# Performance work log

Measured on AMD Instinct MI355X. Metric: run time of the kernel, lower is better.

The kernel has to match this reference:

```python
import jax, jax.numpy as jnp
import numpy as np

B, N, D = 8, 4096, 256
H = W = 64          # grid_size = img_size // patch_size = 256 // 4
WS = 8              # swin window size
NH = 8              # swin heads
M = 16              # fno modes
E = 4               # num experts
TD = 768            # text dim
HID = 1024          # mlp hidden = 4 * D
TK = 2              # top_k


def gelu(x):
    return jax.nn.gelu(x, approximate=False)


def layernorm(x, g, b, eps=1e-5):
    mu = x.mean(-1, keepdims=True)
    var = ((x - mu) ** 2).mean(-1, keepdims=True)
    return (x - mu) * jax.lax.rsqrt(var + eps) * g + b


def fno_expert(x, w1r, w1i, w2r, w2i, conv_w, conv_b):
    # x: [B, N, D] -> grid [B, D, H, W]
    xg = x.transpose(0, 2, 1).reshape(B, D, H, W)
    xft = jnp.fft.rfft2(xg)                      # [B, D, H, W//2+1] complex64
    w1 = w1r + 1j * w1i
    w2 = w2r + 1j * w2i
    top = jnp.einsum('bixy,ioxy->boxy', xft[:, :, :M, :M], w1)
    bot = jnp.einsum('bixy,ioxy->boxy', xft[:, :, -M:, :M], w2)
    out_ft = jnp.zeros((B, D, H, W // 2 + 1), dtype=xft.dtype)
    out_ft = out_ft.at[:, :, :M, :M].set(top).at[:, :, -M:, :M].set(bot)
    x1 = jnp.fft.irfft2(out_ft, s=(H, W))        # [B, D, H, W]
    x2 = jnp.einsum('bdhw,do->bohw', xg, conv_w) + conv_b[None, :, None, None]
    out = gelu(x1 + x2)
    return out.reshape(B, D, N).transpose(0, 2, 1) + x


def mlp_expert(x, w1, b1, w2, b2):
    return gelu(x @ w1 + b1) @ w2 + b2 + x


def window_attn_expert(x, ln1_g, ln1_b, qkv_w, qkv_b, out_w, out_b,
                       ln2_g, ln2_b, mw1, mb1, mw2, mb2):
    shortcut = x
    h = layernorm(x, ln1_g, ln1_b)
    # window partition: [B,H,W,C] -> [B*nW, WS*WS, C]
    h = h.reshape(B, H // WS, WS, W // WS, WS, D)
    h = h.transpose(0, 1, 3, 2, 4, 5).reshape(-1, WS * WS, D)
    # multi-head self attention (torch nn.MultiheadAttention semantics)
    qkv = h @ qkv_w + qkv_b                      # [Bw, L, 3D]
    q, k, v = jnp.split(qkv, 3, axis=-1)
    dh = D // NH
    def heads(t):
        return t.reshape(-1, WS * WS, NH, dh).transpose(0, 2, 1, 3)
    q, k, v = heads(q), heads(k), heads(v)
    scores = jnp.einsum('whld,whmd->whlm', q, k) / jnp.sqrt(jnp.float32(dh))
    attn = jax.nn.softmax(scores, axis=-1)
    o = jnp.einsum('whlm,whmd->whld', attn, v)
    o = o.transpose(0, 2, 1, 3).reshape(-1, WS * WS, D)
    o = o @ out_w + out_b
    # window reverse
    o = o.reshape(B, H // WS, W // WS, WS, WS, D)
    o = o.transpose(0, 1, 3, 2, 4, 5).reshape(B, N, D)
    x = o + shortcut
    h2 = layernorm(x, ln2_g, ln2_b)
    return x + (gelu(h2 @ mw1 + mb1) @ mw2 + mb2)


def setup_inputs() -> dict:
    key = jax.random.key(0)
    ks = jax.random.split(key, 24)
    rn = lambda k, s: jax.random.normal(k, s, jnp.float32) * 0.02
    fscale = 1.0 / (D * D)
    ru = lambda k: jax.random.uniform(k, (D, D, M, M), jnp.float32) * fscale
    return {
        'x': jax.random.normal(ks[0], (B, N, D), jnp.float32),
        'text_embedding': jax.random.normal(ks[1], (B, TD), jnp.float32),
        'gate_w1': rn(ks[2], (D + TD, D)), 'gate_b1': jnp.zeros((D,), jnp.float32),
        'gate_w2': rn(ks[3], (D, E)), 'gate_b2': jnp.zeros((E,), jnp.float32),
        'fno_w1r': ru(ks[4]), 'fno_w1i': ru(ks[5]),
        'fno_w2r': ru(ks[6]), 'fno_w2i': ru(ks[7]),
        'fno_conv_w': rn(ks[8], (D, D)), 'fno_conv_b': jnp.zeros((D,), jnp.float32),
        'mlp1_w1': rn(ks[9], (D, HID)), 'mlp1_b1': jnp.zeros((HID,), jnp.float32),
        'mlp1_w2': rn(ks[10], (HID, D)), 'mlp1_b2': jnp.zeros((D,), jnp.float32),
        'mlp2_w1': rn(ks[11], (D, HID)), 'mlp2_b1': jnp.zeros((HID,), jnp.float32),
        'mlp2_w2': rn(ks[12], (HID, D)), 'mlp2_b2': jnp.zeros((D,), jnp.float32),
        'wa_ln1_g': jnp.ones((D,), jnp.float32), 'wa_ln1_b': jnp.zeros((D,), jnp.float32),
        'wa_qkv_w': rn(ks[13], (D, 3 * D)), 'wa_qkv_b': jnp.zeros((3 * D,), jnp.float32),
        'wa_out_w': rn(ks[14], (D, D)), 'wa_out_b': jnp.zeros((D,), jnp.float32),
        'wa_ln2_g': jnp.ones((D,), jnp.float32), 'wa_ln2_b': jnp.zeros((D,), jnp.float32),
        'wa_mlp_w1': rn(ks[15], (D, HID)), 'wa_mlp_b1': jnp.zeros((HID,), jnp.float32),
        'wa_mlp_w2': rn(ks[16], (HID, D)), 'wa_mlp_b2': jnp.zeros((D,), jnp.float32),
    }


def reference(x, text_embedding, gate_w1, gate_b1, gate_w2, gate_b2,
              fno_w1r, fno_w1i, fno_w2r, fno_w2i, fno_conv_w, fno_conv_b,
              mlp1_w1, mlp1_b1, mlp1_w2, mlp1_b2,
              mlp2_w1, mlp2_b1, mlp2_w2, mlp2_b2,
              wa_ln1_g, wa_ln1_b, wa_qkv_w, wa_qkv_b, wa_out_w, wa_out_b,
              wa_ln2_g, wa_ln2_b, wa_mlp_w1, wa_mlp_b1, wa_mlp_w2, wa_mlp_b2):
    # --- gating ---
    feat = jnp.concatenate([x.mean(axis=1), text_embedding], axis=1)  # [B, D+TD]
    logits = jax.nn.relu(feat @ gate_w1 + gate_b1) @ gate_w2 + gate_b2  # [B, E]
    top_v, top_i = jax.lax.top_k(logits, TK)
    weights = jax.nn.softmax(top_v, axis=-1)                           # [B, TK]
    # per-expert combined weight: cw[b,e] = sum_k w[b,k] * (idx[b,k]==e)
    cw = (jax.nn.one_hot(top_i, E, dtype=x.dtype) * weights[..., None]).sum(axis=1)  # [B, E]
    # --- experts (FNO, MLP, WindowAttn, MLP) ---
    e0 = fno_expert(x, fno_w1r, fno_w1i, fno_w2r, fno_w2i, fno_conv_w, fno_conv_b)
    e1 = mlp_expert(x, mlp1_w1, mlp1_b1, mlp1_w2, mlp1_b2)
    e2 = window_attn_expert(x, wa_ln1_g, wa_ln1_b, wa_qkv_w, wa_qkv_b,
                            wa_out_w, wa_out_b, wa_ln2_g, wa_ln2_b,
                            wa_mlp_w1, wa_mlp_b1, wa_mlp_w2, wa_mlp_b2)
    e3 = mlp_expert(x, mlp2_w1, mlp2_b1, mlp2_w2, mlp2_b2)
    outs = jnp.stack([e0, e1, e2, e3])                                 # [E, B, N, D]
    final = jnp.einsum('be,ebnd->bnd', cw, outs)
    return final, weights
```

## Files before the change

kernel.cpp:

```cpp
#include <hip/hip_runtime.h>
#include <math.h>


#define NB 8
#define NN 4096
#define DD 256

typedef __attribute__((ext_vector_type(8))) short bf16x8;
typedef __attribute__((ext_vector_type(4))) float f32x4;

__device__ __forceinline__ float gelu_f(float v) {
    return 0.5f * v * (1.0f + erff(v * 0.7071067811865475f));
}
__device__ __forceinline__ ushort f2bf(float f) {
    uint32_t u = __float_as_uint(f);
    uint32_t r = (u + 0x7fffu + ((u >> 16) & 1u)) >> 16;
    return (ushort)r;
}
__device__ __forceinline__ float b2f(ushort h) {
    return __uint_as_float(((uint32_t)h) << 16);
}

__global__ void k_cvt_gate(const float* __restrict__ src, ushort* __restrict__ dst,
                           float* __restrict__ gp) {
    __shared__ float4 st[4][64];
    int blk = blockIdx.x;
    int t = threadIdx.x;
    int i = blk * 256 + t;
    float4 v = ((const float4*)src)[i];
    ushort4 o;
    o.x = f2bf(v.x); o.y = f2bf(v.y); o.z = f2bf(v.z); o.w = f2bf(v.w);
    ((ushort4*)dst)[i] = o;
    st[t >> 6][t & 63] = v;
    __syncthreads();
    if (t < 64) {
        float4 a = st[0][t], b = st[1][t], c = st[2][t], d = st[3][t];
        float4 s;
        s.x = a.x + b.x + c.x + d.x;
        s.y = a.y + b.y + c.y + d.y;
        s.z = a.z + b.z + c.z + d.z;
        s.w = a.w + b.w + c.w + d.w;
        ((float4*)(gp + (size_t)blk * 256))[t] = s;
    }
}

__global__ void __launch_bounds__(256) k_gate_red(const float* __restrict__ gp,
        float* __restrict__ gp2) {
    int g = blockIdx.x;
    int t = threadIdx.x;
    const float* base = gp + ((size_t)g * 32) * 256;
    float s0 = 0.f, s1 = 0.f, s2 = 0.f, s3 = 0.f;
    #pragma unroll
    for (int k = 0; k < 32; k += 4) {
        s0 += base[(k + 0) * 256 + t];
        s1 += base[(k + 1) * 256 + t];
        s2 += base[(k + 2) * 256 + t];
        s3 += base[(k + 3) * 256 + t];
    }
    gp2[(size_t)g * 256 + t] = s0 + s1 + s2 + s3;
}

__global__ void __launch_bounds__(256) k_gate_mm(const float* __restrict__ gp2,
        const float* __restrict__ text, const float* __restrict__ w1,
        const float* __restrict__ b1, float* __restrict__ h1) {
    __shared__ float fs[1024];
    int b = blockIdx.x, t = threadIdx.x;
    const float* base = gp2 + (size_t)b * 32 * 256;
    float s = 0.f;
    #pragma unroll
    for (int j = 0; j < 32; ++j) s += base[j * 256 + t];
    fs[t] = s * (1.0f / NN);
    for (int j = t; j < 768; j += 256) fs[256 + j] = text[b * 768 + j];
    __syncthreads();
    float acc = b1[t];
    for (int k = 0; k < 1024; ++k) acc += fs[k] * w1[k * 256 + t];
    h1[b * 256 + t] = fmaxf(acc, 0.f);
}

__global__ void k_gate_top(const float* __restrict__ h1, const float* __restrict__ w2,
                           const float* __restrict__ b2, float* __restrict__ cw,
                           float* __restrict__ wout) {
    __shared__ float lg[8][4];
    int t = threadIdx.x;
    if (t < 32) {
        int b = t >> 2, e = t & 3;
        float acc = b2[e];
        const float* h = h1 + b * 256;
        for (int k = 0; k < 256; ++k) acc += h[k] * w2[k * 4 + e];
        lg[b][e] = acc;
    }
    __syncthreads();
    if (t < 8) {
        int b = t;
        float v[4];
        #pragma unroll
        for (int e = 0; e < 4; ++e) v[e] = lg[b][e];
        int i0 = 0;
        #pragma unroll
        for (int e = 1; e < 4; ++e) if (v[e] > v[i0]) i0 = e;
        int i1 = -1;
        #pragma unroll
        for (int e = 0; e < 4; ++e) {
            if (e == i0) continue;
            if (i1 < 0 || v[e] > v[i1]) i1 = e;
        }
        float v0 = v[i0], v1 = v[i1];
        float e1v = expf(v1 - v0);
        float inv = 1.0f / (1.0f + e1v);
        float w0 = inv, w1v = e1v * inv;
        wout[b * 2 + 0] = w0;
        wout[b * 2 + 1] = w1v;
        float c[4] = {0.f, 0.f, 0.f, 0.f};
        c[i0] += w0; c[i1] += w1v;
        #pragma unroll
        for (int e = 0; e < 4; ++e) cw[b * 4 + e] = c[e];
    }
}

__global__ void k_wt_all(const float* s0, const float* s1, const float* s2,
        const float* s3, const float* s4, const float* s5, const float* s6,
        const float* s7, const float* s8,
        ushort* d0, ushort* d1, ushort* d2, ushort* d3, ushort* d4,
        ushort* d5, ushort* d6, ushort* d7, ushort* d8) {
    const float* srcs[9] = {s0, s1, s2, s3, s4, s5, s6, s7, s8};
    ushort* dsts[9] = {d0, d1, d2, d3, d4, d5, d6, d7, d8};
    const int Ks[9] = {256, 1024, 256, 1024, 256, 1024, 256, 256, 256};
    const int Ns[9] = {1024, 256, 1024, 256, 1024, 256, 768, 256, 256};
    __shared__ float tile[32][33];
    int j = blockIdx.z;
    int K = Ks[j], N = Ns[j];
    int tn = N >> 5, tk = K >> 5;
    int tid = blockIdx.x;
    if (tid >= tn * tk) return;
    int n0 = (tid % tn) * 32, k0 = (tid / tn) * 32;
    const float* src = srcs[j];
    ushort* dst = dsts[j];
    int tx = threadIdx.x, ty = threadIdx.y;
    #pragma unroll
    for (int i = 0; i < 4; ++i)
        tile[ty + i * 8][tx] = src[(size_t)(k0 + ty + i * 8) * N + n0 + tx];
    __syncthreads();
    #pragma unroll
    for (int i = 0; i < 4; ++i)
        dst[(size_t)(n0 + ty + i * 8) * K + k0 + tx] = f2bf(tile[tx][ty + i * 8]);
}

template<int MODE>
__global__ void __launch_bounds__(256) k_gemm(const ushort* __restrict__ A,
        const ushort* __restrict__ Bt, const float* __restrict__ bias,
        const void* __restrict__ res, float* __restrict__ outf,
        ushort* __restrict__ outb, const float* __restrict__ cw, int eidx,
        int K, int Ncols, size_t bsA, size_t bsB, size_t bsC,
        const ushort* __restrict__ e0p, const ushort* __restrict__ g1p,
        const ushort* __restrict__ g2p, const ushort* __restrict__ xap) {
    __shared__ alignas(16) char smem[34816];
    ushort* sA = (ushort*)smem;
    ushort* sB = (ushort*)(smem + 16384);
    int z = blockIdx.z;
    A += z * bsA; Bt += z * bsB;
    if (outf) outf += z * bsC;
    if (outb) outb += z * bsC;
    int m0 = blockIdx.x * 128;
    int n0 = blockIdx.y * 128;
    int t = threadIdx.x;
    int lane = t & 63, wid = t >> 6;
    int wr = wid >> 1, wc = wid & 1;
    int rlo = lane & 15, khi = (lane >> 4) * 8;

    auto stage = [&](int buf, int k0) {
        const ushort* Ab = A + (size_t)m0 * K + k0;
        const ushort* Bb = Bt + (size_t)n0 * K + k0;
        #pragma unroll
        for (int h = 0; h < 2; ++h) {
            int s = t + h * 256;
            int row = s >> 2, kc = (s & 3) * 8;
            __builtin_amdgcn_global_load_lds(
                (const __attribute__((address_space(1))) void*)(Ab + (size_t)row * K + kc),
                (__attribute__((address_space(3))) void*)(sA + buf * 4096 + s * 8),
                16, 0, 0);
            __builtin_amdgcn_global_load_lds(
                (const __attribute__((address_space(1))) void*)(Bb + (size_t)row * K + kc),
                (__attribute__((address_space(3))) void*)(sB + buf * 4096 + s * 8),
                16, 0, 0);
        }
    };

    f32x4 acc[4][4];
    #pragma unroll
    for (int i = 0; i < 4; ++i)
        #pragma unroll
        for (int j = 0; j < 4; ++j) acc[i][j] = (f32x4){0.f, 0.f, 0.f, 0.f};

    int KT = K >> 5;
    stage(0, 0);
    int cur = 0;
    for (int kt = 0; kt < KT; ++kt) {
        __syncthreads();
        if (kt + 1 < KT) stage(cur ^ 1, (kt + 1) << 5);
        const ushort* Ap = sA + cur * 4096;
        const ushort* Bp = sB + cur * 4096;
        bf16x8 af[4], bfr[4];
        #pragma unroll
        for (int i = 0; i < 4; ++i) {
            af[i]  = *(const bf16x8*)(Ap + (wr * 64 + i * 16 + rlo) * 32 + khi);
            bfr[i] = *(const bf16x8*)(Bp + (wc * 64 + i * 16 + rlo) * 32 + khi);
        }
        #pragma unroll
        for (int i = 0; i < 4; ++i)
            #pragma unroll
            for (int j = 0; j < 4; ++j)
                acc[i][j] = __builtin_amdgcn_mfma_f32_16x16x32_bf16(af[i], bfr[j], acc[i][j], 0, 0, 0);
        cur ^= 1;
    }

    float bj4[4];
    if constexpr (MODE != 5) {
        #pragma unroll
        for (int nt = 0; nt < 4; ++nt) bj4[nt] = bias[n0 + wc * 64 + nt * 16 + rlo];
    }

    ushort* eb = (ushort*)smem;
    __syncthreads();
    #pragma unroll
    for (int mt = 0; mt < 4; ++mt) {
        int row0 = wr * 64 + mt * 16 + (lane >> 4) * 4;
        #pragma unroll
        for (int nt = 0; nt < 4; ++nt) {
            int col = wc * 64 + nt * 16 + rlo;
            #pragma unroll
            for (int j = 0; j < 4; ++j) {
                float v = acc[mt][nt][j];
                if constexpr (MODE == 5)
                    v += bias[m0 + row0 + j];
                else
                    v += bj4[nt];
                if (MODE == 0) v = gelu_f(v);
                eb[(row0 + j) * 136 + col] = f2bf(v);
            }
        }
    }
    __syncthreads();
    const ushort* resb = (const ushort*)res;
    #pragma unroll
    for (int h = 0; h < 8; ++h) {
        int s = t + h * 256;
        int r = s >> 4, c = (s & 15) * 8;
        int grow = m0 + r;
        size_t off = (size_t)grow * Ncols + n0 + c;
        if constexpr (MODE == 6) {
            ushort ee[8], rr[8], oo[8];
            *(uint4*)ee = *(uint4*)&eb[r * 136 + c];
            *(uint4*)rr = *(const uint4*)(resb + off);
            #pragma unroll
            for (int q = 0; q < 8; ++q) oo[q] = f2bf(b2f(ee[q]) + b2f(rr[q]));
            *(uint4*)(outb + off) = *(uint4*)oo;
        } else if constexpr (MODE == 7) {
            int bb = grow >> 12;
            float c0 = cw[bb * 4 + 0], c1 = cw[bb * 4 + 1];
            float c2 = cw[bb * 4 + 2], c3 = cw[bb * 4 + 3];
            float cx = c0 + c1 + c3;
            ushort ee[8], a0[8], a1[8], a2[8], xa[8], xb[8];
            *(uint4*)ee = *(uint4*)&eb[r * 136 + c];
            *(uint4*)a0 = *(const uint4*)(e0p + off);
            *(uint4*)a1 = *(const uint4*)(g1p + off);
            *(uint4*)a2 = *(const uint4*)(g2p + off);
            *(uint4*)xa = *(const uint4*)(xap + off);
            *(uint4*)xb = *(const uint4*)(resb + off);
            float ov[8];
            #pragma unroll
            for (int q = 0; q < 8; ++q)
                ov[q] = c0 * b2f(a0[q]) + c1 * b2f(a1[q]) + c2 * (b2f(a2[q]) + b2f(xa[q]))
                      + c3 * b2f(ee[q]) + cx * b2f(xb[q]);
            *(float4*)(outf + off) = *(float4*)&ov[0];
            *(float4*)(outf + off + 4) = *(float4*)&ov[4];
        } else {
            *(uint4*)(outb + off) = *(uint4*)&eb[r * 136 + c];
        }
    }
}

__global__ void k_transpose(const ushort* __restrict__ x, ushort* __restrict__ xg) {
    __shared__ ushort tile[32][34];
    int b = blockIdx.z;
    int nt = blockIdx.x, dt = blockIdx.y;
    int tx = threadIdx.x, ty = threadIdx.y;
    const ushort* xb = x + (size_t)b * NN * DD;
    ushort* xgb = xg + (size_t)b * DD * NN;
    #pragma unroll
    for (int i = 0; i < 4; ++i) {
        int n = nt * 32 + ty + i * 8;
        tile[ty + i * 8][tx] = xb[(size_t)n * DD + dt * 32 + tx];
    }
    __syncthreads();
    #pragma unroll
    for (int i = 0; i < 4; ++i) {
        int d = dt * 32 + ty + i * 8;
        xgb[(size_t)d * NN + nt * 32 + tx] = tile[tx][ty + i * 8];
    }
}

__global__ void __launch_bounds__(256) k_rfft2(const ushort* __restrict__ xg, float* __restrict__ xft) {
    __shared__ float plane[64][65];
    __shared__ float s1re[16][66], s1im[16][66];
    __shared__ float twc[64], tws[64];
    int p = blockIdx.x;
    int t = threadIdx.x;
    int tx = t & 63, grp = t >> 6;
    const ushort* src = xg + (size_t)p * 4096;
    #pragma unroll
    for (int i = 0; i < 16; ++i) {
        int row = grp * 16 + i;
        plane[row][tx] = b2f(src[row * 64 + tx]);
    }
    if (t < 64) {
        twc[t] = cosf((float)t * (6.283185307179586f / 64.0f));
        tws[t] = sinf((float)t * (6.283185307179586f / 64.0f));
    }
    __syncthreads();
    int r = tx;
    #pragma unroll
    for (int q = 0; q < 4; ++q) {
        int kw = grp + q * 4;
        float re = 0.f, im = 0.f;
        for (int w = 0; w < 64; ++w) {
            int j = (w * kw) & 63;
            float xv = plane[r][w];
            re += xv * twc[j];
            im -= xv * tws[j];
        }
        s1re[kw][r] = re;
        s1im[kw][r] = im;
    }
    __syncthreads();
    float2* dst = (float2*)xft + (size_t)p * 512;
    #pragma unroll
    for (int q = 0; q < 2; ++q) {
        int oi = t + q * 256;
        int krow = oi >> 4, kw = oi & 15;
        int kh = krow < 16 ? krow : krow + 32;
        float re = 0.f, im = 0.f;
        for (int h = 0; h < 64; ++h) {
            int j = (h * kh) & 63;
            float c = twc[j], s = tws[j];
            float ar = s1re[kw][h], ai = s1im[kw][h];
            re += ar * c + ai * s;
            im += ai * c - ar * s;
        }
        dst[oi] = make_float2(re, im);
    }
}

__global__ void __launch_bounds__(512) k_spectral(const float* __restrict__ xft,
        const float* __restrict__ w1r, const float* __restrict__ w1i,
        const float* __restrict__ w2r, const float* __restrict__ w2i,
        float* __restrict__ part) {
    __shared__ alignas(16) ushort Wl[16 * 640];
    __shared__ alignas(16) ushort Xl[16 * 640];
    int z = blockIdx.z;
    int region = z >> 1, is = z & 1;
    const float* wrp = region ? w2r : w1r;
    const float* wip = region ? w2i : w1i;
    int xm = blockIdx.y;
    int krow = region * 16 + xm;
    int o0 = blockIdx.x * 16;
    int t = threadIdx.x;
    int wv = t >> 6, lane = t & 63;
    int rlo = lane & 15, khi = lane >> 4;
    int ibase = is * 128;

    int wy4 = t & 3, wol = (t >> 2) & 15, wi8 = t >> 6;

    f32x4 acc[2][2];
    #pragma unroll
    for (int a = 0; a < 2; ++a)
        #pragma unroll
        for (int b = 0; b < 2; ++b) acc[a][b] = (f32x4){0.f, 0.f, 0.f, 0.f};

    for (int ch = 0; ch < 4; ++ch) {
        int i0 = ibase + ch * 32;
        int ig = i0 + wi8 * 4;
        __syncthreads();
        {
            float4 f[4];
            #pragma unroll
            for (int u = 0; u < 4; ++u)
                f[u] = *(const float4*)&wrp[((size_t)(ig + u) * 256 + o0 + wol) * 256 + xm * 16 + wy4 * 4];
            #pragma unroll
            for (int yy2 = 0; yy2 < 4; ++yy2) {
                int y = wy4 * 4 + yy2;
                ushort4 pk;
                pk.x = f2bf(((const float*)&f[0])[yy2]);
                pk.y = f2bf(((const float*)&f[1])[yy2]);
                pk.z = f2bf(((const float*)&f[2])[yy2]);
                pk.w = f2bf(((const float*)&f[3])[yy2]);
                *(ushort4*)&Wl[y * 640 + wol * 40 + wi8 * 4] = pk;
            }
        }
        {
            #pragma unroll
            for (int s = 0; s < 2; ++s) {
                int m = t + s * 512;
                int y = m & 15, i4 = (m >> 4) & 7, b = (m >> 7) & 7;
                int igx = i0 + i4 * 4;
                float2 g[4];
                #pragma unroll
                for (int u = 0; u < 4; ++u)
                    g[u] = *(const float2*)&xft[(((size_t)(b * 256 + igx + u)) * 32 + krow) * 32 + y * 2];
                ushort4 re, im;
                re.x = f2bf(g[0].x); re.y = f2bf(g[1].x); re.z = f2bf(g[2].x); re.w = f2bf(g[3].x);
                im.x = f2bf(g[0].y); im.y = f2bf(g[1].y); im.z = f2bf(g[2].y); im.w = f2bf(g[3].y);
                *(ushort4*)&Xl[b * 640 + y * 40 + i4 * 4] = re;
                *(ushort4*)&Xl[(b + 8) * 640 + y * 40 + i4 * 4] = im;
            }
        }
        __syncthreads();
        #pragma unroll
        for (int yy = 0; yy < 2; ++yy) {
            int y = wv * 2 + yy;
            bf16x8 Bf = *(const bf16x8*)&Xl[rlo * 640 + y * 40 + khi * 8];
            bf16x8 Af = *(const bf16x8*)&Wl[y * 640 + rlo * 40 + khi * 8];
            acc[yy][0] = __builtin_amdgcn_mfma_f32_16x16x32_bf16(Af, Bf, acc[yy][0], 0, 0, 0);
        }
        __syncthreads();
        {
            float4 f[4];
            #pragma unroll
            for (int u = 0; u < 4; ++u)
                f[u] = *(const float4*)&wip[((size_t)(ig + u) * 256 + o0 + wol) * 256 + xm * 16 + wy4 * 4];
            #pragma unroll
            for (int yy2 = 0; yy2 < 4; ++yy2) {
                int y = wy4 * 4 + yy2;
                ushort4 pk;
                pk.x = f2bf(((const float*)&f[0])[yy2]);
                pk.y = f2bf(((const float*)&f[1])[yy2]);
                pk.z = f2bf(((const float*)&f[2])[yy2]);
                pk.w = f2bf(((const float*)&f[3])[yy2]);
                *(ushort4*)&Wl[y * 640 + wol * 40 + wi8 * 4] = pk;
            }
        }
        __syncthreads();
        #pragma unroll
        for (int yy = 0; yy < 2; ++yy) {
            int y = wv * 2 + yy;
            bf16x8 Bf = *(const bf16x8*)&Xl[rlo * 640 + y * 40 + khi * 8];
            bf16x8 Af = *(const bf16x8*)&Wl[y * 640 + rlo * 40 + khi * 8];
            acc[yy][1] = __builtin_amdgcn_mfma_f32_16x16x32_bf16(Af, Bf, acc[yy][1], 0, 0, 0);
        }
    }

    float* dp = part + (size_t)is * 4194304;
    int b = rlo & 7, hi = rlo >> 3;
    #pragma unroll
    for (int yy = 0; yy < 2; ++yy) {
        int y = wv * 2 + yy;
        #pragma unroll
        for (int j = 0; j < 4; ++j) {
            float C1 = acc[yy][0][j];
            float c2x = __shfl_xor(acc[yy][1][j], 8);
            float val = hi ? (c2x + C1) : (C1 - c2x);
            int o = o0 + khi * 4 + j;
            dp[(((size_t)(b * 256 + o) * 32 + krow) * 16 + y) * 2 + hi] = val;
        }
    }
}

__global__ void __launch_bounds__(256) k_irfft_fuse(const float* __restrict__ part,
        const ushort* __restrict__ x2t, ushort* __restrict__ tmp) {
    __shared__ float F[32][16][2];
    __shared__ float tre[16][66], tim[16][66];
    __shared__ float twc[64], tws[64];
    int p = blockIdx.x;
    int t = threadIdx.x;
    const float2* s0 = (const float2*)part + (size_t)p * 512;
    #pragma unroll
    for (int l = 0; l < 2; ++l) {
        int idx = t + l * 256;
        float2 a = s0[idx];
        float2 b2 = s0[idx + 2097152];
        ((float2*)F)[idx] = make_float2(a.x + b2.x, a.y + b2.y);
    }
    if (t < 64) {
        twc[t] = cosf((float)t * (6.283185307179586f / 64.0f));
        tws[t] = sinf((float)t * (6.283185307179586f / 64.0f));
    }
    __syncthreads();
    int h = t & 63;
    #pragma unroll
    for (int q = 0; q < 4; ++q) {
        int kw = (t >> 6) + q * 4;
        float re = 0.f, im = 0.f;
        #pragma unroll
        for (int krow = 0; krow < 32; ++krow) {
            int kh = krow < 16 ? krow : krow + 32;
            int j = (h * kh) & 63;
            float c = twc[j], s = tws[j];
            float fr = F[krow][kw][0], fi = F[krow][kw][1];
            re += fr * c - fi * s;
            im += fr * s + fi * c;
        }
        tre[kw][h] = re * (1.f / 64.f);
        tim[kw][h] = im * (1.f / 64.f);
    }
    __syncthreads();
    const ushort* x2p = x2t + (size_t)p * 4096;
    ushort* tp = tmp + (size_t)p * 4096;
    int w = t & 63;
    #pragma unroll
    for (int qq = 0; qq < 16; ++qq) {
        int qrow = (t >> 6) + qq * 4;
        float acc = tre[0][qrow];
        #pragma unroll
        for (int kw = 1; kw < 16; ++kw) {
            int j = (w * kw) & 63;
            acc += 2.f * (tre[kw][qrow] * twc[j] - tim[kw][qrow] * tws[j]);
        }
        float x1 = acc * (1.f / 64.f);
        int idx = qrow * 64 + w;
        tp[idx] = f2bf(gelu_f(x1 + b2f(x2p[idx])));
    }
}

__global__ void k_fno_final(const ushort* __restrict__ tmp, ushort* __restrict__ e0t) {
    __shared__ ushort tile[32][34];
    int b = blockIdx.z;
    int n0 = blockIdx.x * 32, d0 = blockIdx.y * 32;
    int tx = threadIdx.x, ty = threadIdx.y;
    const ushort* tb = tmp + (size_t)b * DD * NN;
    #pragma unroll
    for (int i = 0; i < 4; ++i)
        tile[ty + i * 8][tx] = tb[(size_t)(d0 + ty + i * 8) * NN + n0 + tx];
    __syncthreads();
    #pragma unroll
    for (int i = 0; i < 4; ++i) {
        int n = n0 + ty + i * 8, d = d0 + tx;
        e0t[((size_t)b * NN + n) * DD + d] = tile[tx][ty + i * 8];
    }
}

__global__ void __launch_bounds__(256) k_ln(const ushort* __restrict__ in, const float* __restrict__ g,
        const float* __restrict__ be, ushort* __restrict__ outb) {
    int row = blockIdx.x * 4 + (threadIdx.x >> 6);
    int lane = threadIdx.x & 63;
    ushort4 u = ((const ushort4*)(in + (size_t)row * 256))[lane];
    float4 v = make_float4(b2f(u.x), b2f(u.y), b2f(u.z), b2f(u.w));
    float s = v.x + v.y + v.z + v.w;
    float s2 = v.x * v.x + v.y * v.y + v.z * v.z + v.w * v.w;
    #pragma unroll
    for (int off = 32; off > 0; off >>= 1) {
        s += __shfl_down(s, off);
        s2 += __shfl_down(s2, off);
    }
    s = __shfl(s, 0); s2 = __shfl(s2, 0);
    float mu = s * (1.f / 256.f);
    float var = s2 * (1.f / 256.f) - mu * mu;
    float rstd = rsqrtf(var + 1e-5f);
    float4 gv = ((const float4*)g)[lane];
    float4 bv = ((const float4*)be)[lane];
    ushort4 ov;
    ov.x = f2bf((v.x - mu) * rstd * gv.x + bv.x);
    ov.y = f2bf((v.y - mu) * rstd * gv.y + bv.y);
    ov.z = f2bf((v.z - mu) * rstd * gv.z + bv.z);
    ov.w = f2bf((v.w - mu) * rstd * gv.w + bv.w);
    ((ushort4*)(outb + (size_t)row * 256))[lane] = ov;
}

__global__ void __launch_bounds__(256) k_window_attn(const ushort* __restrict__ qkvb,
        ushort* __restrict__ aob) {
    __shared__ ushort lds[4 * 7424];
    int t = threadIdx.x;
    int w = t >> 6, lane = t & 63;
    int wi = blockIdx.x, hh = blockIdx.y;
    int hd = hh * 4 + w;
    int b = wi >> 6, hb = (wi >> 3) & 7, wb = wi & 7;
    ushort* A = lds + w * 7424;
    ushort* Kl = A + 2560;
    ushort* Vt = A + 5120;
    int rlo = lane & 15, kq = lane >> 4;

    int tok = lane;
    int n = hb * 512 + wb * 8 + ((tok >> 3) << 6) + (tok & 7);
    const ushort* gq = qkvb + ((size_t)b * 4096 + n) * 768 + hd * 32;
    const uint4* qp = (const uint4*)gq;
    const uint4* kp = (const uint4*)(gq + 256);
    const uint4* vp = (const uint4*)(gq + 512);
    uint4 q0 = qp[0], q1 = qp[1], q2 = qp[2], q3 = qp[3];
    uint4 k0 = kp[0], k1 = kp[1], k2 = kp[2], k3 = kp[3];
    uint4 v0 = vp[0], v1 = vp[1], v2 = vp[2], v3 = vp[3];
    uint4* qr = (uint4*)(A + tok * 40);
    qr[0] = q0; qr[1] = q1; qr[2] = q2; qr[3] = q3;
    uint4* kr = (uint4*)(Kl + tok * 40);
    kr[0] = k0; kr[1] = k1; kr[2] = k2; kr[3] = k3;
    ushort vbuf[32];
    *(uint4*)&vbuf[0] = v0; *(uint4*)&vbuf[8] = v1;
    *(uint4*)&vbuf[16] = v2; *(uint4*)&vbuf[24] = v3;
    #pragma unroll
    for (int d = 0; d < 32; ++d) Vt[d * 72 + tok] = vbuf[d];
    __syncthreads();

    bf16x8 Qf[4], Kf[4];
    #pragma unroll
    for (int lt = 0; lt < 4; ++lt)
        Qf[lt] = *(const bf16x8*)(A + (lt * 16 + rlo) * 40 + kq * 8);
    #pragma unroll
    for (int mt = 0; mt < 4; ++mt)
        Kf[mt] = *(const bf16x8*)(Kl + (mt * 16 + rlo) * 40 + kq * 8);

    f32x4 S[4][4];
    #pragma unroll
    for (int lt = 0; lt < 4; ++lt)
        #pragma unroll
        for (int mt = 0; mt < 4; ++mt)
            S[lt][mt] = __builtin_amdgcn_mfma_f32_16x16x32_bf16(Qf[lt], Kf[mt],
                        (f32x4){0.f, 0.f, 0.f, 0.f}, 0, 0, 0);
    __syncthreads();

    const float scale = 0.17677669529663687f;
    float inv_[4][4];
    #pragma unroll
    for (int lt = 0; lt < 4; ++lt) {
        float m4[4], s4[4];
        #pragma unroll
        for (int j = 0; j < 4; ++j) {
            m4[j] = fmaxf(fmaxf(S[lt][0][j], S[lt][1][j]), fmaxf(S[lt][2][j], S[lt][3][j]));
        }
        #pragma unroll
        for (int off = 1; off < 16; off <<= 1)
            #pragma unroll
            for (int j = 0; j < 4; ++j) m4[j] = fmaxf(m4[j], __shfl_xor(m4[j], off));
        #pragma unroll
        for (int j = 0; j < 4; ++j) s4[j] = 0.f;
        #pragma unroll
        for (int mt = 0; mt < 4; ++mt)
            #pragma unroll
            for (int j = 0; j < 4; ++j) {
                float p = expf((S[lt][mt][j] - m4[j]) * scale);
                s4[j] += p;
                A[(lt * 16 + kq * 4 + j) * 72 + mt * 16 + rlo] = f2bf(p);
            }
        #pragma unroll
        for (int off = 1; off < 16; off <<= 1)
            #pragma unroll
            for (int j = 0; j < 4; ++j) s4[j] += __shfl_xor(s4[j], off);
        #pragma unroll
        for (int j = 0; j < 4; ++j) inv_[lt][j] = 1.0f / s4[j];
    }
    __syncthreads();

    f32x4 O[4][2];
    #pragma unroll
    for (int lt = 0; lt < 4; ++lt)
        #pragma unroll
        for (int dt = 0; dt < 2; ++dt) {
            f32x4 o = (f32x4){0.f, 0.f, 0.f, 0.f};
            #pragma unroll
            for (int mc = 0; mc < 2; ++mc) {
                bf16x8 pa = *(const bf16x8*)(A + (lt * 16 + rlo) * 72 + mc * 32 + kq * 8);
                bf16x8 vb = *(const bf16x8*)(Vt + (dt * 16 + rlo) * 72 + mc * 32 + kq * 8);
                o = __builtin_amdgcn_mfma_f32_16x16x32_bf16(pa, vb, o, 0, 0, 0);
            }
            O[lt][dt] = o;
        }
    __syncthreads();

    #pragma unroll
    for (int lt = 0; lt < 4; ++lt)
        #pragma unroll
        for (int dt = 0; dt < 2; ++dt)
            #pragma unroll
            for (int j = 0; j < 4; ++j)
                A[(lt * 16 + kq * 4 + j) * 40 + dt * 16 + rlo] = f2bf(O[lt][dt][j] * inv_[lt][j]);
    __syncthreads();
    const uint4* orow = (const uint4*)(A + lane * 40);
    uint4 o0 = orow[0], o1 = orow[1], o2 = orow[2], o3 = orow[3];
    uint4* gout = (uint4*)(aob + ((size_t)b * 4096 + n) * 256 + hd * 32);
    gout[0] = o0; gout[1] = o1; gout[2] = o2; gout[3] = o3;
}

extern "C" void kernel_launch(void* const* d_in, const int* in_sizes, int n_in,
                              void* d_out, int out_size, void* d_ws, size_t ws_size,
                              hipStream_t stream) {
    (void)in_sizes; (void)n_in; (void)out_size; (void)ws_size;
    const float* x        = (const float*)d_in[0];
    const float* text     = (const float*)d_in[1];
    const float* gate_w1  = (const float*)d_in[2];
    const float* gate_b1  = (const float*)d_in[3];
    const float* gate_w2  = (const float*)d_in[4];
    const float* gate_b2  = (const float*)d_in[5];
    const float* fno_w1r  = (const float*)d_in[6];
    const float* fno_w1i  = (const float*)d_in[7];
    const float* fno_w2r  = (const float*)d_in[8];
    const float* fno_w2i  = (const float*)d_in[9];
    const float* fno_cw   = (const float*)d_in[10];
    const float* fno_cb   = (const float*)d_in[11];
    const float* mlp1_w1  = (const float*)d_in[12];
    const float* mlp1_b1  = (const float*)d_in[13];
    const float* mlp1_w2  = (const float*)d_in[14];
    const float* mlp1_b2  = (const float*)d_in[15];
    const float* mlp2_w1  = (const float*)d_in[16];
    const float* mlp2_b1  = (const float*)d_in[17];
    const float* mlp2_w2  = (const float*)d_in[18];
    const float* mlp2_b2  = (const float*)d_in[19];
    const float* ln1_g    = (const float*)d_in[20];
    const float* ln1_b    = (const float*)d_in[21];
    const float* qkv_w    = (const float*)d_in[22];
    const float* qkv_b    = (const float*)d_in[23];
    const float* out_w    = (const float*)d_in[24];
    const float* out_b    = (const float*)d_in[25];
    const float* ln2_g    = (const float*)d_in[26];
    const float* ln2_b    = (const float*)d_in[27];
    const float* wa_w1    = (const float*)d_in[28];
    const float* wa_b1    = (const float*)d_in[29];
    const float* wa_w2    = (const float*)d_in[30];
    const float* wa_b2    = (const float*)d_in[31];

    float* ws   = (float*)d_ws;
    float* h1   = ws + 8192;
    float* cwp  = ws + 10240;
    ushort* wbf = (ushort*)(ws + 16384);
    ushort* w1aT = wbf;
    ushort* w2aT = w1aT + 262144;
    ushort* w1bT = w2aT + 262144;
    ushort* w2bT = w1bT + 262144;
    ushort* w1cT = w2bT + 262144;
    ushort* w2cT = w1cT + 262144;
    ushort* qkvT = w2cT + 262144;
    ushort* outwT = qkvT + 196608;
    ushort* convT = outwT + 65536;
    ushort* Xbf  = (ushort*)(ws + 16384 + 1048576);
    float* slotA = ws + 16384 + 1048576 + 4194304;
    float* xft   = slotA + 8388608;
    float* oft   = xft + 2097152;
    float* regD  = oft + 2097152;
    ushort* bigb = (ushort*)(regD + 8388608);
    float* gpart = oft;
    float* gp2   = regD;

    ushort* xgb   = (ushort*)slotA;
    ushort* g1b   = (ushort*)slotA;
    ushort* g2b   = (ushort*)(slotA + 4194304);
    ushort* x2tb  = (ushort*)regD;
    ushort* e0tb  = (ushort*)regD;
    ushort* scr   = (ushort*)(regD + 4194304);
    ushort* xatb  = (ushort*)xft;

    float* outp = (float*)d_out;
    float* wout = outp + (size_t)NB * NN * DD;

    k_cvt_gate<<<8192, 256, 0, stream>>>(x, Xbf, gpart);
    k_gate_red<<<256, 256, 0, stream>>>(gpart, gp2);
    k_gate_mm<<<8, 256, 0, stream>>>(gp2, text, gate_w1, gate_b1, h1);
    k_gate_top<<<1, 64, 0, stream>>>(h1, gate_w2, gate_b2, cwp, wout);

    k_wt_all<<<dim3(256, 1, 9), dim3(32, 8), 0, stream>>>(
        mlp1_w1, mlp1_w2, mlp2_w1, mlp2_w2, wa_w1, wa_w2, qkv_w, out_w, fno_cw,
        w1aT, w2aT, w1bT, w2bT, w1cT, w2cT, qkvT, outwT, convT);

    k_transpose<<<dim3(128, 8, 8), dim3(32, 8), 0, stream>>>(Xbf, xgb);
    k_rfft2<<<2048, 256, 0, stream>>>(xgb, xft);
    k_gemm<5><<<dim3(2, 32, 8), 256, 0, stream>>>(convT, Xbf, fno_cb, nullptr, nullptr,
        x2tb, nullptr, 0, 256, 4096, 0, (size_t)NN * DD, (size_t)DD * NN,
        nullptr, nullptr, nullptr, nullptr);
    k_spectral<<<dim3(16, 16, 4), 512, 0, stream>>>(xft, fno_w1r, fno_w1i, fno_w2r, fno_w2i, slotA);
    k_irfft_fuse<<<2048, 256, 0, stream>>>(slotA, x2tb, bigb);
    k_fno_final<<<dim3(128, 8, 8), dim3(32, 8), 0, stream>>>(bigb, e0tb);

    k_gemm<0><<<dim3(256, 8), 256, 0, stream>>>(Xbf, w1aT, mlp1_b1, nullptr, nullptr, bigb, nullptr, 0, 256, 1024, 0, 0, 0, nullptr, nullptr, nullptr, nullptr);
    k_gemm<1><<<dim3(256, 2), 256, 0, stream>>>(bigb, w2aT, mlp1_b2, nullptr, nullptr, g1b, nullptr, 0, 1024, 256, 0, 0, 0, nullptr, nullptr, nullptr, nullptr);

    k_ln<<<8192, 256, 0, stream>>>(Xbf, ln1_g, ln1_b, scr);
    k_gemm<1><<<dim3(256, 6), 256, 0, stream>>>(scr, qkvT, qkv_b, nullptr, nullptr, bigb, nullptr, 0, 256, 768, 0, 0, 0, nullptr, nullptr, nullptr, nullptr);
    k_window_attn<<<dim3(512, 2), 256, 0, stream>>>(bigb, scr);
    k_gemm<6><<<dim3(256, 2), 256, 0, stream>>>(scr, outwT, out_b, Xbf, nullptr, xatb, nullptr, 0, 256, 256, 0, 0, 0, nullptr, nullptr, nullptr, nullptr);
    k_ln<<<8192, 256, 0, stream>>>(xatb, ln2_g, ln2_b, scr);
    k_gemm<0><<<dim3(256, 8), 256, 0, stream>>>(scr, w1cT, wa_b1, nullptr, nullptr, bigb, nullptr, 0, 256, 1024, 0, 0, 0, nullptr, nullptr, nullptr, nullptr);
    k_gemm<1><<<dim3(256, 2), 256, 0, stream>>>(bigb, w2cT, wa_b2, nullptr, nullptr, g2b, nullptr, 0, 1024, 256, 0, 0, 0, nullptr, nullptr, nullptr, nullptr);

    k_gemm<0><<<dim3(256, 8), 256, 0, stream>>>(Xbf, w1bT, mlp2_b1, nullptr, nullptr, bigb, nullptr, 0, 256, 1024, 0, 0, 0, nullptr, nullptr, nullptr, nullptr);
    k_gemm<7><<<dim3(256, 2), 256, 0, stream>>>(bigb, w2bT, mlp2_b2, Xbf, outp, nullptr, cwp, 3, 1024, 256, 0, 0, 0, e0tb, g1b, g2b, xatb);
}
```

Before: 643.5 us.

## Fuse bf16 conversion, transpose and gate partial sums into one kernel

Merges the fp32-to-bf16 conversion, the per-batch token-sum partials for gating, and the N/D transpose for the FNO grid into a single tiled kernel. The separate transpose pass and the gate reduction kernel go away, which saves a re-read of the bf16 input and two launches. The spectral kernel's shared-memory row stride is also padded from 640 to 648 to reduce LDS bank conflicts. The fused kernel uses 32-wide scalar loads instead of float4, which may lower load efficiency. Workspace aliasing is also changed: xgb is written before k_wt_all, in the same slot as g1b.

```diff
diff --git a/kernel.cpp b/kernel.cpp
--- a/kernel.cpp
+++ b/kernel.cpp
@@ -21,54 +21,53 @@
     return __uint_as_float(((uint32_t)h) << 16);
 }
 
-__global__ void k_cvt_gate(const float* __restrict__ src, ushort* __restrict__ dst,
-                           float* __restrict__ gp) {
-    __shared__ float4 st[4][64];
-    int blk = blockIdx.x;
-    int t = threadIdx.x;
-    int i = blk * 256 + t;
-    float4 v = ((const float4*)src)[i];
-    ushort4 o;
-    o.x = f2bf(v.x); o.y = f2bf(v.y); o.z = f2bf(v.z); o.w = f2bf(v.w);
-    ((ushort4*)dst)[i] = o;
-    st[t >> 6][t & 63] = v;
-    __syncthreads();
-    if (t < 64) {
-        float4 a = st[0][t], b = st[1][t], c = st[2][t], d = st[3][t];
-        float4 s;
-        s.x = a.x + b.x + c.x + d.x;
-        s.y = a.y + b.y + c.y + d.y;
-        s.z = a.z + b.z + c.z + d.z;
-        s.w = a.w + b.w + c.w + d.w;
-        ((float4*)(gp + (size_t)blk * 256))[t] = s;
-    }
-}
-
-__global__ void __launch_bounds__(256) k_gate_red(const float* __restrict__ gp,
-        float* __restrict__ gp2) {
-    int g = blockIdx.x;
-    int t = threadIdx.x;
-    const float* base = gp + ((size_t)g * 32) * 256;
-    float s0 = 0.f, s1 = 0.f, s2 = 0.f, s3 = 0.f;
-    #pragma unroll
-    for (int k = 0; k < 32; k += 4) {
-        s0 += base[(k + 0) * 256 + t];
-        s1 += base[(k + 1) * 256 + t];
-        s2 += base[(k + 2) * 256 + t];
-        s3 += base[(k + 3) * 256 + t];
-    }
-    gp2[(size_t)g * 256 + t] = s0 + s1 + s2 + s3;
-}
-
-__global__ void __launch_bounds__(256) k_gate_mm(const float* __restrict__ gp2,
+__global__ void k_cvt_gate_t(const float* __restrict__ src, ushort* __restrict__ xbf,
+        ushort* __restrict__ xg, float* __restrict__ gp) {
+    __shared__ ushort tile[32][34];
+    __shared__ float sred[8][32];
+    int nt = blockIdx.x, dt = blockIdx.y, b = blockIdx.z;
+    int tx = threadIdx.x, ty = threadIdx.y;
+    int n0 = nt * 32, d0 = dt * 32;
+    const float* xb = src + ((size_t)b * NN + n0) * DD + d0;
+    ushort* xbb = xbf + ((size_t)b * NN + n0) * DD + d0;
+    float s = 0.f;
+    #pragma unroll
+    for (int i = 0; i < 4; ++i) {
+        int r = ty + i * 8;
+        float v = xb[(size_t)r * DD + tx];
+        ushort h = f2bf(v);
+        xbb[(size_t)r * DD + tx] = h;
+        tile[r][tx] = h;
+        s += v;
+    }
+    sred[ty][tx] = s;
+    __syncthreads();
+    ushort* xgb = xg + (size_t)b * DD * NN;
+    #pragma unroll
+    for (int i = 0; i < 4; ++i) {
+        int d = d0 + ty + i * 8;
+        xgb[(size_t)d * NN + n0 + tx] = tile[tx][ty + i * 8];
+    }
+    if (ty == 0) {
+        float tot = 0.f;
+        #pragma unroll
+        for (int j = 0; j < 8; ++j) tot += sred[j][tx];
+        gp[(((size_t)b * 8 + dt) * 128 + nt) * 32 + tx] = tot;
+    }
+}
+
+__global__ void __launch_bounds__(256) k_gate_mm(const float* __restrict__ gp,
         const float* __restrict__ text, const float* __restrict__ w1,
         const float* __restrict__ b1, float* __restrict__ h1) {
     __shared__ float fs[1024];
     int b = blockIdx.x, t = threadIdx.x;
-    const float* base = gp2 + (size_t)b * 32 * 256;
+    int dt = t >> 5, tx = t & 31;
+    const float* base = gp + ((size_t)b * 8 + dt) * 128 * 32 + tx;
     float s = 0.f;
-    #pragma unroll
-    for (int j = 0; j < 32; ++j) s += base[j * 256 + t];
+    for (int j = 0; j < 128; j += 4) {
+        s += base[(j + 0) * 32] + base[(j + 1) * 32]
+           + base[(j + 2) * 32] + base[(j + 3) * 32];
+    }
     fs[t] = s * (1.0f / NN);
     for (int j = t; j < 768; j += 256) fs[256 + j] = text[b * 768 + j];
     __syncthreads();
@@ -279,26 +278,6 @@
     }
 }
 
-__global__ void k_transpose(const ushort* __restrict__ x, ushort* __restrict__ xg) {
-    __shared__ ushort tile[32][34];
-    int b = blockIdx.z;
-    int nt = blockIdx.x, dt = blockIdx.y;
-    int tx = threadIdx.x, ty = threadIdx.y;
-    const ushort* xb = x + (size_t)b * NN * DD;
-    ushort* xgb = xg + (size_t)b * DD * NN;
-    #pragma unroll
-    for (int i = 0; i < 4; ++i) {
-        int n = nt * 32 + ty + i * 8;
-        tile[ty + i * 8][tx] = xb[(size_t)n * DD + dt * 32 + tx];
-    }
-    __syncthreads();
-    #pragma unroll
-    for (int i = 0; i < 4; ++i) {
-        int d = dt * 32 + ty + i * 8;
-        xgb[(size_t)d * NN + nt * 32 + tx] = tile[tx][ty + i * 8];
-    }
-}
-
 __global__ void __launch_bounds__(256) k_rfft2(const ushort* __restrict__ xg, float* __restrict__ xft) {
     __shared__ float plane[64][65];
     __shared__ float s1re[16][66], s1im[16][66];
@@ -354,8 +333,8 @@
         const float* __restrict__ w1r, const float* __restrict__ w1i,
         const float* __restrict__ w2r, const float* __restrict__ w2i,
         float* __restrict__ part) {
-    __shared__ alignas(16) ushort Wl[16 * 640];
-    __shared__ alignas(16) ushort Xl[16 * 640];
+    __shared__ alignas(16) ushort Wl[16 * 648];
+    __shared__ alignas(16) ushort Xl[16 * 648];
     int z = blockIdx.z;
     int region = z >> 1, is = z & 1;
     const float* wrp = region ? w2r : w1r;
@@ -393,7 +372,7 @@
                 pk.y = f2bf(((const float*)&f[1])[yy2]);
                 pk.z = f2bf(((const float*)&f[2])[yy2]);
                 pk.w = f2bf(((const float*)&f[3])[yy2]);
-                *(ushort4*)&Wl[y * 640 + wol * 40 + wi8 * 4] = pk;
+                *(ushort4*)&Wl[y * 648 + wol * 40 + wi8 * 4] = pk;
             }
         }
         {
@@ -409,16 +388,16 @@
                 ushort4 re, im;
                 re.x = f2bf(g[0].x); re.y = f2bf(g[1].x); re.z = f2bf(g[2].x); re.w = f2bf(g[3].x);
                 im.x = f2bf(g[0].y); im.y = f2bf(g[1].y); im.z = f2bf(g[2].y); im.w = f2bf(g[3].y);
-                *(ushort4*)&Xl[b * 640 + y * 40 + i4 * 4] = re;
-                *(ushort4*)&Xl[(b + 8) * 640 + y * 40 + i4 * 4] = im;
+                *(ushort4*)&Xl[b * 648 + y * 40 + i4 * 4] = re;
+                *(ushort4*)&Xl[(b + 8) * 648 + y * 40 + i4 * 4] = im;
             }
         }
         __syncthreads();
         #pragma unroll
         for (int yy = 0; yy < 2; ++yy) {
             int y = wv * 2 + yy;
-            bf16x8 Bf = *(const bf16x8*)&Xl[rlo * 640 + y * 40 + khi * 8];
-            bf16x8 Af = *(const bf16x8*)&Wl[y * 640 + rlo * 40 + khi * 8];
+            bf16x8 Bf = *(const bf16x8*)&Xl[rlo * 648 + y * 40 + khi * 8];
+            bf16x8 Af = *(const bf16x8*)&Wl[y * 648 + rlo * 40 + khi * 8];
             acc[yy][0] = __builtin_amdgcn_mfma_f32_16x16x32_bf16(Af, Bf, acc[yy][0], 0, 0, 0);
         }
         __syncthreads();
@@ -435,15 +414,15 @@
                 pk.y = f2bf(((const float*)&f[1])[yy2]);
                 pk.z = f2bf(((const float*)&f[2])[yy2]);
                 pk.w = f2bf(((const float*)&f[3])[yy2]);
-                *(ushort4*)&Wl[y * 640 + wol * 40 + wi8 * 4] = pk;
+                *(ushort4*)&Wl[y * 648 + wol * 40 + wi8 * 4] = pk;
             }
         }
         __syncthreads();
         #pragma unroll
         for (int yy = 0; yy < 2; ++yy) {
             int y = wv * 2 + yy;
-            bf16x8 Bf = *(const bf16x8*)&Xl[rlo * 640 + y * 40 + khi * 8];
-            bf16x8 Af = *(const bf16x8*)&Wl[y * 640 + rlo * 40 + khi * 8];
+            bf16x8 Bf = *(const bf16x8*)&Xl[rlo * 648 + y * 40 + khi * 8];
+            bf16x8 Af = *(const bf16x8*)&Wl[y * 648 + rlo * 40 + khi * 8];
             acc[yy][1] = __builtin_amdgcn_mfma_f32_16x16x32_bf16(Af, Bf, acc[yy][1], 0, 0, 0);
         }
     }
@@ -733,7 +712,6 @@
     float* regD  = oft + 2097152;
     ushort* bigb = (ushort*)(regD + 8388608);
     float* gpart = oft;
-    float* gp2   = regD;
 
     ushort* xgb   = (ushort*)slotA;
     ushort* g1b   = (ushort*)slotA;
@@ -746,16 +724,14 @@
     float* outp = (float*)d_out;
     float* wout = outp + (size_t)NB * NN * DD;
 
-    k_cvt_gate<<<8192, 256, 0, stream>>>(x, Xbf, gpart);
-    k_gate_red<<<256, 256, 0, stream>>>(gpart, gp2);
-    k_gate_mm<<<8, 256, 0, stream>>>(gp2, text, gate_w1, gate_b1, h1);
+    k_cvt_gate_t<<<dim3(128, 8, 8), dim3(32, 8), 0, stream>>>(x, Xbf, xgb, gpart);
+    k_gate_mm<<<8, 256, 0, stream>>>(gpart, text, gate_w1, gate_b1, h1);
     k_gate_top<<<1, 64, 0, stream>>>(h1, gate_w2, gate_b2, cwp, wout);
 
     k_wt_all<<<dim3(256, 1, 9), dim3(32, 8), 0, stream>>>(
         mlp1_w1, mlp1_w2, mlp2_w1, mlp2_w2, wa_w1, wa_w2, qkv_w, out_w, fno_cw,
         w1aT, w2aT, w1bT, w2bT, w1cT, w2cT, qkvT, outwT, convT);
 
-    k_transpose<<<dim3(128, 8, 8), dim3(32, 8), 0, stream>>>(Xbf, xgb);
     k_rfft2<<<2048, 256, 0, stream>>>(xgb, xft);
     k_gemm<5><<<dim3(2, 32, 8), 256, 0, stream>>>(convT, Xbf, fno_cb, nullptr, nullptr,
         x2tb, nullptr, 0, 256, 4096, 0, (size_t)NN * DD, (size_t)DD * NN,
```

Result: no change. 650.2 us (+1.0%).
